# Optimization experiments

Measured on AMD Instinct MI355X. Metric: run time of the kernel, lower is better.

The kernel has to match this reference:

```python
import jax, jax.numpy as jnp
import numpy as np

B, D, K, N = 32, 512, 64, 1024
EPS = 1e-12  # torch F.normalize eps


def setup_inputs() -> dict:
    key = jax.random.key(0)
    k1, k2, k3 = jax.random.split(key, 3)
    x = jax.random.normal(k1, (B, D, N), dtype=jnp.float32)
    conv_w = jax.random.normal(k2, (K, D), dtype=jnp.float32) * (1.0 / np.sqrt(D))
    centers = jax.random.normal(k3, (D, K), dtype=jnp.float32)
    return {"x": x, "conv_w": conv_w, "centers": centers}


def reference(x, conv_w, centers):
    # scores: 1x1 conv over flattened spatial dim -> [B, K, N]
    scores = jnp.einsum('kd,bdn->bkn', conv_w, x)
    assign = jax.nn.softmax(scores, axis=1)                 # softmax over clusters
    # Algebraic rewrite of sum_n assign[b,k,n] * (x[b,d,n] - centers[d,k]):
    vlad = (jnp.einsum('bdn,bkn->bdk', x, assign)
            - centers[None, :, :] * assign.sum(axis=-1)[:, None, :])  # [B, D, K]
    # intra-normalization over descriptor dim D (F.normalize with eps clamp)
    vlad = vlad / jnp.maximum(jnp.linalg.norm(vlad, axis=1, keepdims=True), EPS)
    desc = vlad.reshape(vlad.shape[0], -1)                  # [B, D*K]
    desc = desc / jnp.maximum(jnp.linalg.norm(desc, axis=1, keepdims=True), EPS)
    return desc
```

## Files before the change

kernel.cpp:

```cpp
#include <hip/hip_runtime.h>
#include <hip/hip_bf16.h>

#define Bv 32
#define Dv 512
#define Kv 64
#define Nv 1024
#define EPSv 1e-12f

typedef __attribute__((ext_vector_type(8))) short bf16x8;
typedef __attribute__((ext_vector_type(4))) float f32x4;

__device__ __forceinline__ unsigned short f2b(float f) {
  union { float f; unsigned u; } v; v.f = f;
  unsigned r = v.u + 0x7fffu + ((v.u >> 16) & 1u);
  return (unsigned short)(r >> 16);
}
__device__ __forceinline__ unsigned pack2(float a, float b) {
  return (unsigned)f2b(a) | ((unsigned)f2b(b) << 16);
}
__device__ __forceinline__ unsigned cvtpk(float a, float b) {
  unsigned r;
  asm("v_cvt_pk_bf16_f32 %0, %1, %2" : "=v"(r) : "v"(a), "v"(b));
  return r;
}

#define GLOAD_LDS16(gsrc, ldst)                                             \
  __builtin_amdgcn_global_load_lds(                                         \
      (const __attribute__((address_space(1))) void*)(gsrc),                \
      (__attribute__((address_space(3))) void*)(ldst), 16, 0, 0)

__global__ __launch_bounds__(256) void wconv(const float* __restrict__ w,
                                             unsigned short* __restrict__ wbf,
                                             float* __restrict__ zbuf) {
  int id = blockIdx.x * 256 + threadIdx.x;
  int i = id * 4;
  float4 v = *(const float4*)&w[i];
  uint2 o = make_uint2(pack2(v.x, v.y), pack2(v.z, v.w));
  *(uint2*)&wbf[i] = o;
  if (id < 2 * Bv * Kv) zbuf[id] = 0.f;
}

__global__ __launch_bounds__(512) void fused_scores(
    const float* __restrict__ x, const unsigned short* __restrict__ wbf,
    unsigned short* __restrict__ assign, float* __restrict__ asum) {
  __shared__ unsigned short xT[64 * 520];
  __shared__ float redmax[4][64];
  __shared__ float redsum[4][64];

  const int t = threadIdx.x;
  const int flat = blockIdx.x;
  const int i0 = flat >> 3;
  const int b = (flat & 7) + 8 * (i0 & 3);
  const int nt = i0 >> 2;
  const int n0 = nt * 64;

  {
    const int lo = t & 15;
    const int hi = t >> 4;
    const int s = (lo >> 1) & 3;
    const float* xb = x + (size_t)b * Dv * Nv + n0 + lo * 4;
    float4 xr0[4], xr1[4];

#define FS_ISSUE(slot, r)                                                     \
  {                                                                           \
    const float* _s = xb + (size_t)((hi + 32 * (r)) * 2) * Nv;                \
    asm volatile("global_load_dwordx4 %0, %1, off"                            \
                 : "=v"(xr0[slot]) : "v"(_s));                                \
    asm volatile("global_load_dwordx4 %0, %1, off"                            \
                 : "=v"(xr1[slot]) : "v"(_s + Nv));                           \
  }

    FS_ISSUE(0, 0) FS_ISSUE(1, 1) FS_ISSUE(2, 2) FS_ISSUE(3, 3)
    __builtin_amdgcn_sched_barrier(0);

#pragma unroll
    for (int r = 0; r < 8; r++) {
      const int nout = (r < 5) ? 6 : (14 - 2 * r);
      asm volatile("s_waitcnt vmcnt(%0)" :: "i"(nout));
      __builtin_amdgcn_sched_barrier(0);
      float4 v0 = xr0[r & 3];
      float4 v1 = xr1[r & 3];
      int d = (hi + 32 * r) * 2;
      int n4 = lo * 4;
      unsigned w0 = pack2(v0.x, v1.x);
      unsigned w1 = pack2(v0.y, v1.y);
      unsigned w2 = pack2(v0.z, v1.z);
      unsigned w3 = pack2(v0.w, v1.w);
      unsigned a0 = (s & 1) ? w1 : w0, a1 = (s & 1) ? w2 : w1,
               a2 = (s & 1) ? w3 : w2, a3 = (s & 1) ? w0 : w3;
      unsigned b0 = (s & 2) ? a2 : a0, b1 = (s & 2) ? a3 : a1,
               b2 = (s & 2) ? a0 : a2, b3 = (s & 2) ? a1 : a3;
      *(unsigned*)&xT[(n4 + ((0 + s) & 3)) * 520 + d] = b0;
      *(unsigned*)&xT[(n4 + ((1 + s) & 3)) * 520 + d] = b1;
      *(unsigned*)&xT[(n4 + ((2 + s) & 3)) * 520 + d] = b2;
      *(unsigned*)&xT[(n4 + ((3 + s) & 3)) * 520 + d] = b3;
      if (r < 4) FS_ISSUE(r & 3, r + 4)
      __builtin_amdgcn_sched_barrier(0);
    }
#undef FS_ISSUE
  }
  __syncthreads();

  const int wv = t >> 6;
  const int lane = t & 63;
  const int q = lane >> 4;
  const int m = lane & 15;
  const int k16 = wv & 3;
  const int nsub = wv >> 2;

  f32x4 acc0 = {0.f, 0.f, 0.f, 0.f};
  f32x4 acc1 = {0.f, 0.f, 0.f, 0.f};

  const unsigned short* wp = wbf + (size_t)(k16 * 16 + m) * Dv + q * 8;
  const unsigned short* l0 = &xT[(nsub * 32 + m) * 520 + q * 8];
  const unsigned short* l1 = l0 + 16 * 520;

#pragma unroll
  for (int d0 = 0; d0 < Dv; d0 += 32) {
    bf16x8 af = *(const bf16x8*)(wp + d0);
    bf16x8 bf0 = *(const bf16x8*)(l0 + d0);
    bf16x8 bf1 = *(const bf16x8*)(l1 + d0);
    acc0 = __builtin_amdgcn_mfma_f32_16x16x32_bf16(af, bf0, acc0, 0, 0, 0);
    acc1 = __builtin_amdgcn_mfma_f32_16x16x32_bf16(af, bf1, acc1, 0, 0, 0);
  }

  float m0 = fmaxf(fmaxf(acc0[0], acc0[1]), fmaxf(acc0[2], acc0[3]));
  float m1 = fmaxf(fmaxf(acc1[0], acc1[1]), fmaxf(acc1[2], acc1[3]));
  m0 = fmaxf(m0, __shfl_xor(m0, 16)); m0 = fmaxf(m0, __shfl_xor(m0, 32));
  m1 = fmaxf(m1, __shfl_xor(m1, 16)); m1 = fmaxf(m1, __shfl_xor(m1, 32));
  if (q == 0) {
    redmax[k16][nsub * 32 + m] = m0;
    redmax[k16][nsub * 32 + 16 + m] = m1;
  }
  __syncthreads();
  const int c0 = nsub * 32 + m, c1 = c0 + 16;
  float mc0 = fmaxf(fmaxf(redmax[0][c0], redmax[1][c0]), fmaxf(redmax[2][c0], redmax[3][c0]));
  float mc1 = fmaxf(fmaxf(redmax[0][c1], redmax[1][c1]), fmaxf(redmax[2][c1], redmax[3][c1]));

  float e0[4], e1[4];
  float s0 = 0.f, s1 = 0.f;
#pragma unroll
  for (int r = 0; r < 4; r++) {
    e0[r] = __expf(acc0[r] - mc0); s0 += e0[r];
    e1[r] = __expf(acc1[r] - mc1); s1 += e1[r];
  }
  s0 += __shfl_xor(s0, 16); s0 += __shfl_xor(s0, 32);
  s1 += __shfl_xor(s1, 16); s1 += __shfl_xor(s1, 32);
  if (q == 0) {
    redsum[k16][c0] = s0;
    redsum[k16][c1] = s1;
  }
  __syncthreads();
  float sc0 = 1.0f / (redsum[0][c0] + redsum[1][c0] + redsum[2][c0] + redsum[3][c0]);
  float sc1 = 1.0f / (redsum[0][c1] + redsum[1][c1] + redsum[2][c1] + redsum[3][c1]);

  unsigned short* at_ = assign + ((size_t)b * 16 + nt) * (Kv * 64)
                        + (size_t)(k16 * 16 + q * 4) * 64 + nsub * 32;
#pragma unroll
  for (int r = 0; r < 4; r++) {
    float v0 = e0[r] * sc0;
    float v1 = e1[r] * sc1;
    at_[r * 64 + m] = f2b(v0);
    at_[r * 64 + 16 + m] = f2b(v1);
    float p = v0 + v1;
    p += __shfl_xor(p, 1); p += __shfl_xor(p, 2);
    p += __shfl_xor(p, 4); p += __shfl_xor(p, 8);
    if (m == 0) atomicAdd(&asum[b * Kv + k16 * 16 + q * 4 + r], p);
  }
}

__global__ __launch_bounds__(256) void vlad_stage(
    const float* __restrict__ x, const unsigned short* __restrict__ assign,
    const float* __restrict__ centers, const float* __restrict__ asum,
    float* __restrict__ vlad, float* __restrict__ colsq) {
  __shared__ float xsf[2][2][2048];
  __shared__ unsigned short as_[2][2][4096];

  const int t = threadIdx.x;
  const int flat = blockIdx.x;
  const int i0 = flat >> 3;
  const int b = (flat & 7) + 8 * (i0 & 3);
  const int dg = i0 >> 2;

  const int w = t >> 6;
  const int dh = w & 1;
  const int kh = w >> 1;
  const int lane = t & 63;
  const int q = lane >> 4;
  const int m = lane & 15;

  const int rs = lane >> 3;
  const int csw_a = (lane & 7) ^ (rs & 7);
  const int rx = lane >> 4;

  const float* xdg = x + ((size_t)b * Dv + dg * 32) * Nv;
  const unsigned short* abase = assign + (size_t)b * 16 * (Kv * 64);

#define STAGE(buf, rr)                                                        \
  {                                                                           \
    _Pragma("unroll")                                                         \
    for (int s = 0; s < 2; s++) {                                             \
      int tile = (rr) * 2 + s;                                                \
      _Pragma("unroll")                                                       \
      for (int i = 0; i < 2; i++) {                                           \
        int dl = w * 8 + i * 4 + rx;                   \
        const float* _xs = xdg + (size_t)dl * Nv + tile * 64                  \
                           + (((lane & 15) ^ (dl & 7)) * 4);                  \
        GLOAD_LDS16(_xs, &xsf[buf][s][(w * 8 + i * 4) * 64]);                 \
      }                                                                       \
      const unsigned short* _a1 = abase + (size_t)tile * (Kv * 64)            \
                                  + (w * 16 + rs) * 64 + csw_a * 8;           \
      GLOAD_LDS16(_a1, &as_[buf][s][w * 1024]);                               \
      GLOAD_LDS16(_a1 + 512, &as_[buf][s][w * 1024 + 512]);                   \
    }                                                                         \
  }

  f32x4 acc0 = {0.f,0.f,0.f,0.f}, acc1 = {0.f,0.f,0.f,0.f};

  STAGE(0, 0)
  STAGE(1, 1)
  asm volatile("s_waitcnt vmcnt(8)");
  __builtin_amdgcn_sched_barrier(0);
  __builtin_amdgcn_s_barrier();
  __builtin_amdgcn_sched_barrier(0);

  const int row = dh * 16 + m;
  const int mk7 = m & 7;
#pragma unroll
  for (int rr = 0; rr < 8; rr++) {
    const int buf = rr & 1;
#pragma unroll
    for (int s = 0; s < 2; s++) {
#pragma unroll
      for (int nc = 0; nc < 2; nc++) {
        const int c0 = nc * 8 + q * 2;
        float4 f0 = *(const float4*)&xsf[buf][s][row * 64 + ((c0 ^ mk7)) * 4];
        float4 f1 = *(const float4*)&xsf[buf][s][row * 64 + (((c0 + 1) ^ mk7)) * 4];
        bf16x8 xv;
        unsigned* xu = (unsigned*)&xv;
        xu[0] = cvtpk(f0.x, f0.y);
        xu[1] = cvtpk(f0.z, f0.w);
        xu[2] = cvtpk(f1.x, f1.y);
        xu[3] = cvtpk(f1.z, f1.w);
        const int cidx = ((nc * 4 + q) ^ mk7) * 8;
        bf16x8 a0 = *(const bf16x8*)&as_[buf][s][(kh * 32 + m) * 64 + cidx];
        bf16x8 a1 = *(const bf16x8*)&as_[buf][s][(kh * 32 + 16 + m) * 64 + cidx];
        acc0 = __builtin_amdgcn_mfma_f32_16x16x32_bf16(xv, a0, acc0, 0, 0, 0);
        acc1 = __builtin_amdgcn_mfma_f32_16x16x32_bf16(xv, a1, acc1, 0, 0, 0);
      }
    }
    if (rr < 7) {
      __builtin_amdgcn_sched_barrier(0);
      __builtin_amdgcn_s_barrier();
      __builtin_amdgcn_sched_barrier(0);
      if (rr < 6) {
        STAGE(buf, rr + 2)
        asm volatile("s_waitcnt vmcnt(8)");
      } else {
        asm volatile("s_waitcnt vmcnt(0)");
      }
      __builtin_amdgcn_sched_barrier(0);
      __builtin_amdgcn_s_barrier();
      __builtin_amdgcn_sched_barrier(0);
    }
  }
#undef STAGE

  const int k0 = kh * 32 + m;
  const int k1 = k0 + 16;
  const float as0 = asum[b * Kv + k0];
  const float as1 = asum[b * Kv + k1];
  float ss0 = 0.f, ss1 = 0.f;
#pragma unroll
  for (int r = 0; r < 4; r++) {
    int d = dg * 32 + dh * 16 + q * 4 + r;
    float v0 = acc0[r] - centers[d * Kv + k0] * as0;
    float v1 = acc1[r] - centers[d * Kv + k1] * as1;
    vlad[((size_t)b * Dv + d) * Kv + k0] = v0;
    vlad[((size_t)b * Dv + d) * Kv + k1] = v1;
    ss0 = fmaf(v0, v0, ss0);
    ss1 = fmaf(v1, v1, ss1);
  }
  ss0 += __shfl_xor(ss0, 16); ss0 += __shfl_xor(ss0, 32);
  ss1 += __shfl_xor(ss1, 16); ss1 += __shfl_xor(ss1, 32);
  if (q == 0) {
    atomicAdd(&colsq[b * Kv + k0], ss0);
    atomicAdd(&colsq[b * Kv + k1], ss1);
  }
}

__global__ __launch_bounds__(256) void scale_kernel(
    const float* __restrict__ vlad, const float* __restrict__ colsq,
    float* __restrict__ out) {
  const int t = threadIdx.x;
  const size_t i = ((size_t)blockIdx.x * 256 + t) * 4;
  const int b = (int)(i >> 15);
  __shared__ float scs[64];
  __shared__ float bsh;
  if (t < 64) {
    float tot = colsq[b * Kv + t];
    float sc = 1.0f / fmaxf(sqrtf(tot), EPSv);
    scs[t] = sc;
    float contrib = tot * sc * sc;
#pragma unroll
    for (int off = 32; off > 0; off >>= 1) contrib += __shfl_down(contrib, off);
    if (t == 0) bsh = 1.0f / fmaxf(sqrtf(contrib), EPSv);
  }
  __syncthreads();
  float4 v = *(const float4*)&vlad[i];
  const int k = (int)(i & 63);
  float4 o;
  o.x = v.x * scs[k + 0] * bsh;
  o.y = v.y * scs[k + 1] * bsh;
  o.z = v.z * scs[k + 2] * bsh;
  o.w = v.w * scs[k + 3] * bsh;
  *(float4*)&out[i] = o;
}

extern "C" void kernel_launch(void* const* d_in, const int* in_sizes, int n_in,
                              void* d_out, int out_size, void* d_ws, size_t ws_size,
                              hipStream_t stream) {
  const float* x = (const float*)d_in[0];
  const float* w = (const float*)d_in[1];
  const float* centers = (const float*)d_in[2];
  float* out = (float*)d_out;

  char* ws = (char*)d_ws;
  unsigned short* assign = (unsigned short*)ws;
  float* vlad = (float*)(ws + 4194304);
  unsigned short* wbf = (unsigned short*)(ws + 8388608);
  float* asum = (float*)(ws + 8454144);
  float* colsq = asum + Bv * Kv;

  wconv<<<32, 256, 0, stream>>>(w, wbf, asum);
  fused_scores<<<512, 512, 0, stream>>>(x, wbf, assign, asum);
  vlad_stage<<<512, 256, 0, stream>>>(x, assign, centers, asum, vlad, colsq);
  scale_kernel<<<1024, 256, 0, stream>>>(vlad, colsq, out);
}
```

Baseline: 122.4 us.

## Fuse final normalization into vlad_stage via cooperative grid sync

Merges the scale kernel into vlad_stage. The kernel is launched cooperatively, and after the column-norm atomics a grid-wide sync lets each block apply intra- and global normalization to its register-held results before writing the output directly. This removes the intermediate vlad buffer write and reread plus one kernel launch. In exchange it adds a grid barrier, and it requires all 512 blocks to be co-resident, which launch_bounds(256,2) is meant to help with.

```diff
diff --git a/kernel.cpp b/kernel.cpp
--- a/kernel.cpp
+++ b/kernel.cpp
@@ -1,5 +1,6 @@
 #include <hip/hip_runtime.h>
 #include <hip/hip_bf16.h>
+#include <hip/hip_cooperative_groups.h>
 
 #define Bv 32
 #define Dv 512
@@ -169,12 +170,14 @@
   }
 }
 
-__global__ __launch_bounds__(256) void vlad_stage(
+__global__ __launch_bounds__(256, 2) void vlad_stage(
     const float* __restrict__ x, const unsigned short* __restrict__ assign,
     const float* __restrict__ centers, const float* __restrict__ asum,
-    float* __restrict__ vlad, float* __restrict__ colsq) {
+    float* __restrict__ out, float* __restrict__ colsq) {
   __shared__ float xsf[2][2][2048];
   __shared__ unsigned short as_[2][2][4096];
+  __shared__ float scs[64];
+  __shared__ float bshs;
 
   const int t = threadIdx.x;
   const int flat = blockIdx.x;
@@ -270,16 +273,15 @@
   const int k1 = k0 + 16;
   const float as0 = asum[b * Kv + k0];
   const float as1 = asum[b * Kv + k1];
+  float v0a[4], v1a[4];
   float ss0 = 0.f, ss1 = 0.f;
 #pragma unroll
   for (int r = 0; r < 4; r++) {
     int d = dg * 32 + dh * 16 + q * 4 + r;
-    float v0 = acc0[r] - centers[d * Kv + k0] * as0;
-    float v1 = acc1[r] - centers[d * Kv + k1] * as1;
-    vlad[((size_t)b * Dv + d) * Kv + k0] = v0;
-    vlad[((size_t)b * Dv + d) * Kv + k1] = v1;
-    ss0 = fmaf(v0, v0, ss0);
-    ss1 = fmaf(v1, v1, ss1);
+    v0a[r] = acc0[r] - centers[d * Kv + k0] * as0;
+    v1a[r] = acc1[r] - centers[d * Kv + k1] * as1;
+    ss0 = fmaf(v0a[r], v0a[r], ss0);
+    ss1 = fmaf(v1a[r], v1a[r], ss1);
   }
   ss0 += __shfl_xor(ss0, 16); ss0 += __shfl_xor(ss0, 32);
   ss1 += __shfl_xor(ss1, 16); ss1 += __shfl_xor(ss1, 32);
@@ -287,16 +289,9 @@
     atomicAdd(&colsq[b * Kv + k0], ss0);
     atomicAdd(&colsq[b * Kv + k1], ss1);
   }
-}
-
-__global__ __launch_bounds__(256) void scale_kernel(
-    const float* __restrict__ vlad, const float* __restrict__ colsq,
-    float* __restrict__ out) {
-  const int t = threadIdx.x;
-  const size_t i = ((size_t)blockIdx.x * 256 + t) * 4;
-  const int b = (int)(i >> 15);
-  __shared__ float scs[64];
-  __shared__ float bsh;
+
+  cooperative_groups::this_grid().sync();
+
   if (t < 64) {
     float tot = colsq[b * Kv + t];
     float sc = 1.0f / fmaxf(sqrtf(tot), EPSv);
@@ -304,17 +299,18 @@
     float contrib = tot * sc * sc;
 #pragma unroll
     for (int off = 32; off > 0; off >>= 1) contrib += __shfl_down(contrib, off);
-    if (t == 0) bsh = 1.0f / fmaxf(sqrtf(contrib), EPSv);
+    if (t == 0) bshs = 1.0f / fmaxf(sqrtf(contrib), EPSv);
   }
   __syncthreads();
-  float4 v = *(const float4*)&vlad[i];
-  const int k = (int)(i & 63);
-  float4 o;
-  o.x = v.x * scs[k + 0] * bsh;
-  o.y = v.y * scs[k + 1] * bsh;
-  o.z = v.z * scs[k + 2] * bsh;
-  o.w = v.w * scs[k + 3] * bsh;
-  *(float4*)&out[i] = o;
+  const float bsh = bshs;
+  const float c0s = scs[k0] * bsh;
+  const float c1s = scs[k1] * bsh;
+#pragma unroll
+  for (int r = 0; r < 4; r++) {
+    int d = dg * 32 + dh * 16 + q * 4 + r;
+    out[((size_t)b * Dv + d) * Kv + k0] = v0a[r] * c0s;
+    out[((size_t)b * Dv + d) * Kv + k1] = v1a[r] * c1s;
+  }
 }
 
 extern "C" void kernel_launch(void* const* d_in, const int* in_sizes, int n_in,
@@ -327,13 +323,15 @@
 
   char* ws = (char*)d_ws;
   unsigned short* assign = (unsigned short*)ws;
-  float* vlad = (float*)(ws + 4194304);
-  unsigned short* wbf = (unsigned short*)(ws + 8388608);
-  float* asum = (float*)(ws + 8454144);
+  unsigned short* wbf = (unsigned short*)(ws + 4194304);
+  float* asum = (float*)(ws + 4259840);
   float* colsq = asum + Bv * Kv;
 
   wconv<<<32, 256, 0, stream>>>(w, wbf, asum);
   fused_scores<<<512, 512, 0, stream>>>(x, wbf, assign, asum);
-  vlad_stage<<<512, 256, 0, stream>>>(x, assign, centers, asum, vlad, colsq);
-  scale_kernel<<<1024, 256, 0, stream>>>(vlad, colsq, out);
-}
+
+  void* vsargs[] = {(void*)&x, (void*)&assign, (void*)&centers,
+                    (void*)&asum, (void*)&out, (void*)&colsq};
+  hipLaunchCooperativeKernel(reinterpret_cast<void*>(vlad_stage),
+                             dim3(512), dim3(256), vsargs, 0, stream);
+}
```

Measured after the change: 199.1 us. +62.7%, slower.
